# Performance work log

Hardware: AMD Instinct MI355X
Metric: run time of the kernel (lower is better)

The kernel has to match this reference:

```python
import jax, jax.numpy as jnp
import numpy as np

B, Wd, C, H, F = 48, 88, 256, 32, 1024
NH_SELF, NH_CROSS = 8, 8


def _ln(x, g, b, eps=1e-5):
    mu = x.mean(-1, keepdims=True)
    var = ((x - mu) ** 2).mean(-1, keepdims=True)
    return (x - mu) / jnp.sqrt(var + eps) * g + b


def setup_inputs() -> dict:
    key = jax.random.key(0)
    ks = jax.random.split(key, 16)
    s = 0.02  # weight init scale
    d = {
        'pooled_features': jax.random.normal(ks[0], (B, Wd, C), jnp.float32),
        'features': jax.random.normal(ks[1], (B, C, H, Wd), jnp.float32),
        'self_pe': jax.random.normal(ks[2], (Wd, C), jnp.float32),
        'cross_pe': jax.random.normal(ks[3], (H, C), jnp.float32),
    }
    # LayerNorm params
    for n in ['ln_qs', 'ln_vs', 'ln_qc', 'ln_kv', 'ln_vc', 'ln_ffn']:
        d[n + '_g'] = jnp.ones((C,), jnp.float32)
        d[n + '_b'] = jnp.zeros((C,), jnp.float32)
    # attention projections (stored [in,out]; y = x @ W + b)
    names = ['Wq_s', 'Wk_s', 'Wv_s', 'Wp_s', 'Wq_c', 'Wk_c', 'Wv_c', 'Wp_c']
    for i, n in enumerate(names):
        d[n] = jax.random.normal(ks[4 + i], (C, C), jnp.float32) * s
    for n in ['bq_s', 'bv_s', 'bp_s', 'bq_c', 'bv_c', 'bp_c']:
        d[n] = jnp.zeros((C,), jnp.float32)
    # FFN
    d['W1'] = jax.random.normal(ks[12], (C, F), jnp.float32) * s
    d['b1'] = jnp.zeros((F,), jnp.float32)
    d['W2'] = jax.random.normal(ks[13], (F, C), jnp.float32) * s
    d['b2'] = jnp.zeros((C,), jnp.float32)
    return d


def reference(pooled_features, features, self_pe, cross_pe,
              ln_qs_g, ln_qs_b, ln_vs_g, ln_vs_b,
              ln_qc_g, ln_qc_b, ln_kv_g, ln_kv_b, ln_vc_g, ln_vc_b,
              ln_ffn_g, ln_ffn_b,
              Wq_s, bq_s, Wk_s, Wv_s, bv_s, Wp_s, bp_s,
              Wq_c, bq_c, Wk_c, Wv_c, bv_c, Wp_c, bp_c,
              W1, b1, W2, b2):
    b, w, c = pooled_features.shape
    h = features.shape[2]
    ds = c // NH_SELF
    dc = c // NH_CROSS

    # ---- cross attention first (op_order='cross_first', with_pe=True) ----
    xq = pooled_features                                  # [B,W,C]
    qn = _ln(xq, ln_qc_g, ln_qc_b)
    kv = jnp.transpose(features, (0, 3, 2, 1))            # [B,W,H,C]
    kn = _ln(kv + cross_pe[None, None], ln_kv_g, ln_kv_b)
    vn = _ln(kv, ln_vc_g, ln_vc_b)
    q = (qn @ Wq_c + bq_c).reshape(b, w, NH_CROSS, dc)    # query len 1 per column
    k = (kn @ Wk_c).reshape(b, w, h, NH_CROSS, dc)
    v = (vn @ Wv_c + bv_c).reshape(b, w, h, NH_CROSS, dc)
    attn = jnp.einsum('bwhd,bwkhd->bwhk', q, k) * (dc ** -0.5)
    attn = jax.nn.softmax(attn, axis=-1)
    out = jnp.einsum('bwhk,bwkhd->bwhd', attn, v).reshape(b, w, c)
    x = out @ Wp_c + bp_c + xq

    # ---- self attention over width tokens ----
    qn = _ln(x + self_pe[None], ln_qs_g, ln_qs_b)
    vn = _ln(x, ln_vs_g, ln_vs_b)
    q = (qn @ Wq_s + bq_s).reshape(b, w, NH_SELF, ds)
    k = (qn @ Wk_s).reshape(b, w, NH_SELF, ds)
    v = (vn @ Wv_s + bv_s).reshape(b, w, NH_SELF, ds)
    attn = jnp.einsum('bnhd,bmhd->bhnm', q, k) * (ds ** -0.5)
    attn = jax.nn.softmax(attn, axis=-1)
    out = jnp.einsum('bhnm,bmhd->bnhd', attn, v).reshape(b, w, c)
    x = out @ Wp_s + bp_s + x

    # ---- FFN (mmcv FFN, num_fcs=2, GELU, identity residual) ----
    hdn = _ln(x, ln_ffn_g, ln_ffn_b)
    hdn = jax.nn.gelu(hdn @ W1 + b1, approximate=False) @ W2 + b2
    return x + hdn
```

## Files before the change

kernel.cpp:

```cpp
#include <hip/hip_runtime.h>
#include <math.h>

#define B_   48
#define W_   88
#define C_   256
#define H_   32
#define F_   1024
#define BW_  (B_ * W_)
#define BWH_ (B_ * W_ * H_)
#define HW_  (H_ * W_)

typedef float  f32x4  __attribute__((ext_vector_type(4)));
typedef __bf16 bf16x8 __attribute__((ext_vector_type(8)));

__device__ __forceinline__ unsigned short f2bf(float f) {
  union { float f; unsigned int u; } v; v.f = f;
  unsigned int r = v.u + 0x7FFFu + ((v.u >> 16) & 1u);
  return (unsigned short)(r >> 16);
}
__device__ __forceinline__ float bf2f(unsigned short h) {
  union { unsigned int u; float f; } v; v.u = ((unsigned int)h) << 16;
  return v.f;
}
__device__ __forceinline__ unsigned int pack2(float a, float b) {
  return (unsigned int)f2bf(a) | ((unsigned int)f2bf(b) << 16);
}

__global__ __launch_bounds__(256) void prep_all(
    const float* __restrict__ Wq_s, const float* __restrict__ Wk_s,
    const float* __restrict__ Wv_s, const float* __restrict__ Wp_s,
    const float* __restrict__ W1, const float* __restrict__ W2,
    const float* __restrict__ Wq_c, const float* __restrict__ Wk_c,
    const float* __restrict__ Wv_c, const float* __restrict__ Wp_c,
    const float* __restrict__ bq_s, const float* __restrict__ bv_s,
    const float* __restrict__ bq_c, const float* __restrict__ bv_c,
    const float* __restrict__ bp_c,
    const float* __restrict__ pooled, const float* __restrict__ cross_pe,
    const float* __restrict__ ln_qc_g, const float* __restrict__ ln_qc_b,
    unsigned short* __restrict__ wqkvs, unsigned short* __restrict__ wps,
    unsigned short* __restrict__ w1t, unsigned short* __restrict__ w2t,
    unsigned short* __restrict__ mqk, unsigned short* __restrict__ mvp,
    float* __restrict__ bqk, float* __restrict__ bvp,
    float* __restrict__ bqkvs, float* __restrict__ spe,
    unsigned short* __restrict__ qn_c) {
  __shared__ float smem[256 * 33 + 4 * 33];
  int blk = blockIdx.x, t = threadIdx.x;

  if (blk < 768) {
    const float* src; unsigned short* dst; int Cc, R, tile;
    if (blk < 64)       { src = Wq_s; dst = wqkvs;          Cc = 256;  R = 256;  tile = blk; }
    else if (blk < 128) { src = Wk_s; dst = wqkvs + 65536;  Cc = 256;  R = 256;  tile = blk - 64; }
    else if (blk < 192) { src = Wv_s; dst = wqkvs + 131072; Cc = 256;  R = 256;  tile = blk - 128; }
    else if (blk < 256) { src = Wp_s; dst = wps;            Cc = 256;  R = 256;  tile = blk - 192; }
    else if (blk < 512) { src = W1;   dst = w1t;            Cc = 1024; R = 256;  tile = blk - 256; }
    else                { src = W2;   dst = w2t;            Cc = 256;  R = 1024; tile = blk - 512; }
    int tcn = Cc >> 5;
    int tr = tile / tcn, tc = tile % tcn;
    float (*lds)[33] = (float(*)[33])smem;
    int r = t >> 3, c4 = (t & 7) * 4;
    float4 v = *(const float4*)(src + (size_t)(tr * 32 + r) * Cc + tc * 32 + c4);
    lds[r][c4 + 0] = v.x; lds[r][c4 + 1] = v.y; lds[r][c4 + 2] = v.z; lds[r][c4 + 3] = v.w;
    __syncthreads();
    int rd = t >> 3, cd4 = (t & 7) * 4;
    uint2 u;
    u.x = pack2(lds[cd4 + 0][rd], lds[cd4 + 1][rd]);
    u.y = pack2(lds[cd4 + 2][rd], lds[cd4 + 3][rd]);
    *(uint2*)(dst + (size_t)(tc * 32 + rd) * R + tr * 32 + cd4) = u;
  } else if (blk < 1280) {
    int lb = blk - 768;
    int h = lb >> 6, cb = lb & 63;
    float (*wq)[33] = (float(*)[33])smem;
    float (*wk)[33] = (float(*)[33])(smem + 256 * 33);
#pragma unroll
    for (int p = 0; p < 8; p++) {
      int dp = (t >> 3) + 32 * p, d4 = (t & 7) * 4;
      float4 v = *(const float4*)(Wq_c + (size_t)dp * 256 + 32 * h + d4);
      wq[dp][d4 + 0] = v.x; wq[dp][d4 + 1] = v.y; wq[dp][d4 + 2] = v.z; wq[dp][d4 + 3] = v.w;
    }
    if (t < 128) {
      int c_l = t >> 5, dd = t & 31;
      wk[c_l][dd] = Wk_c[(size_t)(cb * 4 + c_l) * 256 + 32 * h + dd];
    }
    __syncthreads();
    const float scale = 0.17677669529663689f;
    int c_l = t >> 6, ln = t & 63;
    int n = 256 * h + cb * 4 + c_l;
#pragma unroll
    for (int j = 0; j < 4; j++) {
      int dp = ln + 64 * j;
      float acc = 0.f;
#pragma unroll
      for (int dd = 0; dd < 32; dd++) acc += wq[dp][dd] * wk[c_l][dd];
      mqk[(size_t)n * 256 + dp] = f2bf(acc * scale);
    }
    if (ln == 0) {
      float bb = 0.f;
#pragma unroll
      for (int dd = 0; dd < 32; dd++) bb += bq_c[32 * h + dd] * wk[c_l][dd];
      bqk[n] = bb * scale;
    }
  } else if (blk < 1792) {
    int lb = blk - 1280;
    int h = lb >> 6, db = lb & 63;
    float (*wv)[33] = (float(*)[33])smem;
    float (*wp)[33] = (float(*)[33])(smem + 256 * 33);
#pragma unroll
    for (int p = 0; p < 8; p++) {
      int c = (t >> 3) + 32 * p, d4 = (t & 7) * 4;
      float4 v = *(const float4*)(Wv_c + (size_t)c * 256 + 32 * h + d4);
      wv[c][d4 + 0] = v.x; wv[c][d4 + 1] = v.y; wv[c][d4 + 2] = v.z; wv[c][d4 + 3] = v.w;
    }
    if (t < 128) {
      int d_l = t >> 5, dd = t & 31;
      wp[d_l][dd] = Wp_c[(size_t)(32 * h + dd) * 256 + db * 4 + d_l];
    }
    __syncthreads();
    int d_l = t >> 6, ln = t & 63;
    int d = db * 4 + d_l;
#pragma unroll
    for (int j = 0; j < 4; j++) {
      int c = ln + 64 * j;
      float acc = 0.f;
#pragma unroll
      for (int dd = 0; dd < 32; dd++) acc += wv[c][dd] * wp[d_l][dd];
      mvp[(size_t)d * 2048 + 256 * h + c] = f2bf(acc);
    }
  } else if (blk == 1792) {
    float acc = bp_c[t];
    for (int dp = 0; dp < 256; dp++) acc += bv_c[dp] * Wp_c[(size_t)dp * 256 + t];
    bvp[t] = acc;
    bqkvs[t] = bq_s[t]; bqkvs[256 + t] = 0.f; bqkvs[512 + t] = bv_s[t];
  } else if (blk == 1793) {
    int j = t >> 3, cp = t & 7;
    float sp = 0.f, sp2 = 0.f;
    for (int i = 0; i < 32; i++) {
      float v = cross_pe[j * 256 + cp * 32 + i];
      sp += v; sp2 += v * v;
    }
    smem[j * 8 + cp] = sp; smem[256 + j * 8 + cp] = sp2;
    __syncthreads();
    if (t < 32) {
      float a = 0.f, a2 = 0.f;
      for (int i = 0; i < 8; i++) { a += smem[t * 8 + i]; a2 += smem[256 + t * 8 + i]; }
      spe[t] = a; spe[32 + t] = a2;
    }
  } else {
    int row = blk - 1794, c = t;
    float v = pooled[(size_t)row * C_ + c];
    float s1 = v, s2 = v * v;
#pragma unroll
    for (int m = 32; m > 0; m >>= 1) {
      s1 += __shfl_xor(s1, m, 64); s2 += __shfl_xor(s2, m, 64);
    }
    float* red = smem;
    int wave = c >> 6;
    if ((c & 63) == 0) { red[wave] = s1; red[4 + wave] = s2; }
    __syncthreads();
    s1 = red[0] + red[1] + red[2] + red[3];
    s2 = red[4] + red[5] + red[6] + red[7];
    float mu = s1 * (1.f / C_);
    float rs = rsqrtf(s2 * (1.f / C_) - mu * mu + 1e-5f);
    qn_c[(size_t)row * C_ + c] = f2bf((v - mu) * rs * ln_qc_g[c] + ln_qc_b[c]);
  }
}

__global__ __launch_bounds__(704) void xattn_score(
    const float* __restrict__ features, const unsigned short* __restrict__ qt,
    const float* __restrict__ gk, const float* __restrict__ cross_pe,
    unsigned short* __restrict__ part1, float* __restrict__ pstat) {
  int b = blockIdx.x >> 4, ch = blockIdx.x & 15, c0 = ch * 16;
  __shared__ unsigned short kvl[2][16 * 8 * 88];
  __shared__ float pel[32][16];
  int t = threadIdx.x, w = t >> 3, head = t & 7;
  if (t < 512) {
    int j = t >> 4, c = t & 15;
    pel[j][c] = cross_pe[j * 256 + c0 + c];
  }
  float gq[16];
  {
    const unsigned short* qrow = qt + (size_t)(b * 88 + w) * 2048 + head * 256 + c0;
    bf16x8 q0 = *(const bf16x8*)qrow;
    bf16x8 q1 = *(const bf16x8*)(qrow + 8);
#pragma unroll
    for (int i = 0; i < 8; i++) {
      gq[i]     = gk[c0 + i]     * (float)q0[i];
      gq[8 + i] = gk[c0 + 8 + i] * (float)q1[i];
    }
  }
  const float* fbase = features + (size_t)(b * 256 + c0) * HW_;
  float4 rg[4];
  int iA[4];
  auto loadq = [&](int q) {
#pragma unroll
    for (int k = 0; k < 4; k++) {
      int p4 = t + k * 704;
      int c = p4 / 176, r = p4 - c * 176;
      int j8 = r / 22, w4 = (r - j8 * 22) * 4;
      iA[k] = c * 704 + j8 * 88 + w4;
      rg[k] = *(const float4*)(fbase + (size_t)c * HW_ + (q * 8 + j8) * 88 + w4);
    }
  };
  auto storeq = [&](int buf) {
#pragma unroll
    for (int k = 0; k < 4; k++) {
      uint2 u;
      u.x = pack2(rg[k].x, rg[k].y);
      u.y = pack2(rg[k].z, rg[k].w);
      *(uint2*)&kvl[buf][iA[k]] = u;
    }
  };
  unsigned short* dst = part1 + (size_t)((b * 16 + ch) * 88 + w) * 256;
  loadq(0); storeq(0);
  __syncthreads();
  for (int q = 0; q < 4; q++) {
    int cur = q & 1;
    if (q < 3) loadq(q + 1);
    const unsigned short* kb = kvl[cur];
    float a1q[8];
#pragma unroll
    for (int i = 0; i < 8; i++) a1q[i] = 0.f;
#pragma unroll
    for (int c = 0; c < 16; c++) {
      float g = gq[c];
      const unsigned short* row = kb + c * 704 + w;
#pragma unroll
      for (int j8 = 0; j8 < 8; j8++)
        a1q[j8] += g * (bf2f(row[j8 * 88]) + pel[q * 8 + j8][c]);
    }
    {
      float s1 = 0.f, s2 = 0.f, cr = 0.f;
#pragma unroll
      for (int c = 0; c < 16; c++) {
        float v = bf2f(kb[c * 704 + head * 88 + w]);
        s1 += v; s2 += v * v; cr += v * pel[q * 8 + head][c];
      }
      size_t sb = (size_t)(b * 16 + ch) * 3 * 2816 + (q * 8 + head) * 88 + w;
      pstat[sb] = s1; pstat[sb + 2816] = s2; pstat[sb + 5632] = cr;
    }
    {
      unsigned short pk[8];
#pragma unroll
      for (int i = 0; i < 8; i++) pk[i] = f2bf(a1q[i]);
      *(uint4*)(dst + q * 64 + head * 8) = *(uint4*)pk;
    }
    if (q < 3) storeq(cur ^ 1);
    __syncthreads();
  }
}

__global__ __launch_bounds__(256) void xattn_sm(
    const unsigned short* __restrict__ part1, const float* __restrict__ pstat,
    const unsigned short* __restrict__ qt, const float* __restrict__ spe,
    const float* __restrict__ gk, const float* __restrict__ bk,
    float* __restrict__ pr, float* __restrict__ s2a) {
  int bw = blockIdx.x, b = bw / 88, w = bw - b * 88;
  int t = threadIdx.x, head = t >> 5, j = t & 31;
  __shared__ float statl[3][32];
  int pidx = ((j >> 3) << 6) + head * 8 + (j & 7);
  float a1 = 0.f;
  for (int ch = 0; ch < 16; ch++)
    a1 += bf2f(part1[(size_t)((b * 16 + ch) * 88 + w) * 256 + pidx]);
  if (t < 96) {
    int s = t >> 5, jj = t & 31;
    float v = 0.f;
    for (int ch = 0; ch < 16; ch++)
      v += pstat[(size_t)(b * 16 + ch) * 3 * 2816 + s * 2816 + jj * 88 + w];
    statl[s][jj] = v;
  }
  __syncthreads();
  float s1 = statl[0][j], s2v = statl[1][j], cr = statl[2][j];
  float mu  = s1 * (1.f / 256.f);
  float rs  = rsqrtf(s2v * (1.f / 256.f) - mu * mu + 1e-5f);
  float muk = (s1 + spe[j]) * (1.f / 256.f);
  float rsk = rsqrtf((s2v + 2.f * cr + spe[32 + j]) * (1.f / 256.f) - muk * muk + 1e-5f);
  float a3 = 0.f, a4 = 0.f;
  {
    const unsigned short* qrow = qt + (size_t)bw * 2048 + head * 256 + j * 8;
#pragma unroll
    for (int i = 0; i < 8; i++) {
      int c = j * 8 + i;
      float qv = bf2f(qrow[i]);
      a3 += bk[c] * qv; a4 += gk[c] * qv;
    }
  }
#pragma unroll
  for (int m = 16; m > 0; m >>= 1) { a3 += __shfl_xor(a3, m, 32); a4 += __shfl_xor(a4, m, 32); }
  float s = rsk * a1 + a3 - muk * rsk * a4;
  float mx = s;
#pragma unroll
  for (int m = 16; m > 0; m >>= 1) mx = fmaxf(mx, __shfl_xor(mx, m, 32));
  float e = __expf(s - mx);
  float sum = e;
#pragma unroll
  for (int m = 16; m > 0; m >>= 1) sum += __shfl_xor(sum, m, 32);
  float p = e / sum;
  pr[((size_t)bw * 8 + head) * 32 + j] = p * rs;
  float sp = p * rs * mu;
#pragma unroll
  for (int m = 16; m > 0; m >>= 1) sp += __shfl_xor(sp, m, 32);
  if (j == 0) s2a[(size_t)bw * 8 + head] = sp;
}

__global__ __launch_bounds__(704) void xattn_ctx(
    const float* __restrict__ features, const float* __restrict__ pr,
    const float* __restrict__ s2a, const float* __restrict__ gv,
    const float* __restrict__ bvv, unsigned short* __restrict__ ctx) {
  int b = blockIdx.x >> 4, ch = blockIdx.x & 15, c0 = ch * 16;
  __shared__ unsigned short kvl[2][16 * 8 * 88];
  int t = threadIdx.x, w = t >> 3, head = t & 7;
  float S2 = s2a[(size_t)(b * 88 + w) * 8 + head];
  float U[16];
#pragma unroll
  for (int i = 0; i < 16; i++) U[i] = 0.f;

  const float* fbase = features + (size_t)(b * 256 + c0) * HW_;
  const float* prbase = pr + ((size_t)(b * 88 + w) * 8 + head) * 32;
  float4 rg[4];
  int iA[4];
  auto loadq = [&](int q) {
#pragma unroll
    for (int k = 0; k < 4; k++) {
      int p4 = t + k * 704;
      int c = p4 / 176, r = p4 - c * 176;
      int j8 = r / 22, w4 = (r - j8 * 22) * 4;
      iA[k] = c * 704 + j8 * 88 + w4;
      rg[k] = *(const float4*)(fbase + (size_t)c * HW_ + (q * 8 + j8) * 88 + w4);
    }
  };
  auto storeq = [&](int buf) {
#pragma unroll
    for (int k = 0; k < 4; k++) {
      uint2 u;
      u.x = pack2(rg[k].x, rg[k].y);
      u.y = pack2(rg[k].z, rg[k].w);
      *(uint2*)&kvl[buf][iA[k]] = u;
    }
  };
  loadq(0); storeq(0);
  __syncthreads();
  for (int q = 0; q < 4; q++) {
    int cur = q & 1;
    if (q < 3) loadq(q + 1);
    const unsigned short* kb = kvl[cur];
    float4 p0 = *(const float4*)(prbase + q * 8);
    float4 p1 = *(const float4*)(prbase + q * 8 + 4);
    float prr8[8] = {p0.x, p0.y, p0.z, p0.w, p1.x, p1.y, p1.z, p1.w};
#pragma unroll
    for (int c = 0; c < 16; c++) {
      const unsigned short* row = kb + c * 704 + w;
      float acc = U[c];
#pragma unroll
      for (int j8 = 0; j8 < 8; j8++)
        acc += prr8[j8] * bf2f(row[j8 * 88]);
      U[c] = acc;
    }
    if (q < 3) storeq(cur ^ 1);
    __syncthreads();
  }
  unsigned short* orow = ctx + (size_t)(b * 88 + w) * 2048 + head * 256 + c0;
  unsigned short pk[16];
#pragma unroll
  for (int i = 0; i < 16; i++)
    pk[i] = f2bf(gv[c0 + i] * (U[i] - S2) + bvv[c0 + i]);
  *(uint4*)(orow) = *(uint4*)pk;
  *(uint4*)(orow + 8) = *(uint4*)(pk + 8);
}

__global__ __launch_bounds__(256) void ln_rows(
    const float* __restrict__ x,
    const float* __restrict__ g, const float* __restrict__ bta,
    unsigned short* __restrict__ out) {
  int row = blockIdx.x, c = threadIdx.x;
  float v = x[(size_t)row * C_ + c];
  float s1 = v, s2 = v * v;
#pragma unroll
  for (int m = 32; m > 0; m >>= 1) {
    s1 += __shfl_xor(s1, m, 64);
    s2 += __shfl_xor(s2, m, 64);
  }
  __shared__ float red[8];
  int wave = c >> 6;
  if ((c & 63) == 0) { red[wave] = s1; red[4 + wave] = s2; }
  __syncthreads();
  s1 = red[0] + red[1] + red[2] + red[3];
  s2 = red[4] + red[5] + red[6] + red[7];
  float mu = s1 * (1.f / C_);
  float rs = rsqrtf(s2 * (1.f / C_) - mu * mu + 1e-5f);
  out[(size_t)row * C_ + c] = f2bf((v - mu) * rs * g[c] + bta[c]);
}

__global__ __launch_bounds__(256) void ln_dual(
    const float* __restrict__ x, const float* __restrict__ pe,
    const float* __restrict__ g1, const float* __restrict__ b1a,
    const float* __restrict__ g2, const float* __restrict__ b2a,
    unsigned short* __restrict__ out1, unsigned short* __restrict__ out2) {
  int row = blockIdx.x, c = threadIdx.x;
  float v = x[(size_t)row * C_ + c];
  float vp = v + pe[(size_t)(row % 88) * C_ + c];
  float s1 = v, s2 = v * v, t1 = vp, t2 = vp * vp;
#pragma unroll
  for (int m = 32; m > 0; m >>= 1) {
    s1 += __shfl_xor(s1, m, 64); s2 += __shfl_xor(s2, m, 64);
    t1 += __shfl_xor(t1, m, 64); t2 += __shfl_xor(t2, m, 64);
  }
  __shared__ float red[16];
  int wave = c >> 6;
  if ((c & 63) == 0) {
    red[wave] = s1; red[4 + wave] = s2; red[8 + wave] = t1; red[12 + wave] = t2;
  }
  __syncthreads();
  s1 = red[0] + red[1] + red[2] + red[3];
  s2 = red[4] + red[5] + red[6] + red[7];
  t1 = red[8] + red[9] + red[10] + red[11];
  t2 = red[12] + red[13] + red[14] + red[15];
  float mu = s1 * (1.f / C_), rs = rsqrtf(s2 * (1.f / C_) - mu * mu + 1e-5f);
  float mup = t1 * (1.f / C_), rsp = rsqrtf(t2 * (1.f / C_) - mup * mup + 1e-5f);
  out1[(size_t)row * C_ + c] = f2bf((vp - mup) * rsp * g1[c] + b1a[c]);
  out2[(size_t)row * C_ + c] = f2bf((v - mu) * rs * g2[c] + b2a[c]);
}

__global__ __launch_bounds__(256) void gemm_bt(
    const unsigned short* __restrict__ A, const unsigned short* __restrict__ Bt,
    int M, int N, int K,
    const float* __restrict__ bias, const float* __restrict__ resid,
    float* __restrict__ outF, unsigned short* __restrict__ outB, int act_gelu) {
  __shared__ __attribute__((aligned(16))) unsigned short As[64][32];
  __shared__ __attribute__((aligned(16))) unsigned short Bs[64][32];
  const int tiles_n = N >> 6;
  const int bm = blockIdx.x / tiles_n;
  const int bn = blockIdx.x % tiles_n;
  const int tid = threadIdx.x;
  const int wave = tid >> 6, lane = tid & 63;
  const int quad = lane >> 4, lr = lane & 15;
  const int wm = (wave >> 1) << 5, wn = (wave & 1) << 5;
  const int lrow = tid >> 2;
  const int lcol = (tid & 3) << 3;
  const size_t a_base = (size_t)(bm * 64 + lrow) * K + lcol;
  const size_t b_base = (size_t)(bn * 64 + lrow) * K + lcol;
  f32x4 acc[2][2] = {};
  uint4 areg = *(const uint4*)(A + a_base);
  uint4 breg = *(const uint4*)(Bt + b_base);
  for (int k0 = 0; k0 < K; k0 += 32) {
    *(uint4*)&As[lrow][lcol] = areg;
    *(uint4*)&Bs[lrow][lcol] = breg;
    __syncthreads();
    if (k0 + 32 < K) {
      areg = *(const uint4*)(A + a_base + k0 + 32);
      breg = *(const uint4*)(Bt + b_base + k0 + 32);
    }
    bf16x8 af0 = *(const bf16x8*)&As[wm + lr][quad << 3];
    bf16x8 af1 = *(const bf16x8*)&As[wm + 16 + lr][quad << 3];
    bf16x8 bf0 = *(const bf16x8*)&Bs[wn + lr][quad << 3];
    bf16x8 bf1 = *(const bf16x8*)&Bs[wn + 16 + lr][quad << 3];
    acc[0][0] = __builtin_amdgcn_mfma_f32_16x16x32_bf16(af0, bf0, acc[0][0], 0, 0, 0);
    acc[0][1] = __builtin_amdgcn_mfma_f32_16x16x32_bf16(af0, bf1, acc[0][1], 0, 0, 0);
    acc[1][0] = __builtin_amdgcn_mfma_f32_16x16x32_bf16(af1, bf0, acc[1][0], 0, 0, 0);
    acc[1][1] = __builtin_amdgcn_mfma_f32_16x16x32_bf16(af1, bf1, acc[1][1], 0, 0, 0);
    __syncthreads();
  }
#pragma unroll
  for (int i = 0; i < 2; i++)
#pragma unroll
    for (int j = 0; j < 2; j++)
#pragma unroll
      for (int rr = 0; rr < 4; rr++) {
        int row = bm * 64 + wm + i * 16 + quad * 4 + rr;
        int col = bn * 64 + wn + j * 16 + lr;
        float val = acc[i][j][rr];
        if (bias) val += bias[col];
        if (act_gelu) val = 0.5f * val * (1.f + erff(val * 0.70710678118654752f));
        if (resid) val += resid[(size_t)row * N + col];
        if (outF) outF[(size_t)row * N + col] = val;
        else outB[(size_t)row * N + col] = f2bf(val);
      }
}

__global__ __launch_bounds__(256) void gemm_bt_st(
    const unsigned short* __restrict__ A, const unsigned short* __restrict__ Bt,
    int M, int N, int K, int ldc,
    const float* __restrict__ bias, float* __restrict__ outF) {
  __shared__ __attribute__((aligned(16))) unsigned short As[64][32];
  __shared__ __attribute__((aligned(16))) unsigned short Bs[64][32];
  const int tiles_n = N >> 6;
  const int bm = blockIdx.x / tiles_n;
  const int bn = blockIdx.x % tiles_n;
  const int tid = threadIdx.x;
  const int wave = tid >> 6, lane = tid & 63;
  const int quad = lane >> 4, lr = lane & 15;
  const int wm = (wave >> 1) << 5, wn = (wave & 1) << 5;
  const int lrow = tid >> 2;
  const int lcol = (tid & 3) << 3;
  const size_t a_base = (size_t)(bm * 64 + lrow) * K + lcol;
  const size_t b_base = (size_t)(bn * 64 + lrow) * K + lcol;
  f32x4 acc[2][2] = {};
  uint4 areg = *(const uint4*)(A + a_base);
  uint4 breg = *(const uint4*)(Bt + b_base);
  for (int k0 = 0; k0 < K; k0 += 32) {
    *(uint4*)&As[lrow][lcol] = areg;
    *(uint4*)&Bs[lrow][lcol] = breg;
    __syncthreads();
    if (k0 + 32 < K) {
      areg = *(const uint4*)(A + a_base + k0 + 32);
      breg = *(const uint4*)(Bt + b_base + k0 + 32);
    }
    bf16x8 af0 = *(const bf16x8*)&As[wm + lr][quad << 3];
    bf16x8 af1 = *(const bf16x8*)&As[wm + 16 + lr][quad << 3];
    bf16x8 bf0 = *(const bf16x8*)&Bs[wn + lr][quad << 3];
    bf16x8 bf1 = *(const bf16x8*)&Bs[wn + 16 + lr][quad << 3];
    acc[0][0] = __builtin_amdgcn_mfma_f32_16x16x32_bf16(af0, bf0, acc[0][0], 0, 0, 0);
    acc[0][1] = __builtin_amdgcn_mfma_f32_16x16x32_bf16(af0, bf1, acc[0][1], 0, 0, 0);
    acc[1][0] = __builtin_amdgcn_mfma_f32_16x16x32_bf16(af1, bf0, acc[1][0], 0, 0, 0);
    acc[1][1] = __builtin_amdgcn_mfma_f32_16x16x32_bf16(af1, bf1, acc[1][1], 0, 0, 0);
    __syncthreads();
  }
#pragma unroll
  for (int i = 0; i < 2; i++)
#pragma unroll
    for (int j = 0; j < 2; j++)
#pragma unroll
      for (int rr = 0; rr < 4; rr++) {
        int row = bm * 64 + wm + i * 16 + quad * 4 + rr;
        int col = bn * 64 + wn + j * 16 + lr;
        outF[(size_t)row * ldc + col] = acc[i][j][rr] + bias[col];
      }
}

__global__ __launch_bounds__(192) void self_attn3(
    const float* __restrict__ qkv, unsigned short* __restrict__ out) {
  int b = blockIdx.x >> 3;
  int h = blockIdx.x & 7;
  int t = threadIdx.x;
  __shared__ float kl[88][33];
  __shared__ float vl[88][33];
  for (int i = t; i < 704; i += 192) {
    int m = i >> 3, d4 = (i & 7) << 2;
    float4 kv4 = *(const float4*)(qkv + (size_t)(b * 88 + m) * 768 + 256 + h * 32 + d4);
    float4 vv4 = *(const float4*)(qkv + (size_t)(b * 88 + m) * 768 + 512 + h * 32 + d4);
    kl[m][d4 + 0] = kv4.x; kl[m][d4 + 1] = kv4.y; kl[m][d4 + 2] = kv4.z; kl[m][d4 + 3] = kv4.w;
    vl[m][d4 + 0] = vv4.x; vl[m][d4 + 1] = vv4.y; vl[m][d4 + 2] = vv4.z; vl[m][d4 + 3] = vv4.w;
  }
  __syncthreads();
  int r = t >> 1, dh = t & 1;
  if (r < 88) {
    const float* qrow = qkv + (size_t)(b * 88 + r) * 768 + h * 32;
    float qr[32];
#pragma unroll
    for (int g = 0; g < 8; g++) {
      float4 q4 = *(const float4*)(qrow + g * 4);
      qr[g * 4 + 0] = q4.x; qr[g * 4 + 1] = q4.y; qr[g * 4 + 2] = q4.z; qr[g * 4 + 3] = q4.w;
    }
    float sreg[44];
    float mx = -1e30f;
    int m0 = dh * 44;
    for (int mi = 0; mi < 44; mi++) {
      const float* krow = kl[m0 + mi];
      float s = 0.f;
#pragma unroll
      for (int d = 0; d < 32; d++) s += qr[d] * krow[d];
      s *= 0.17677669529663689f;
      sreg[mi] = s;
      mx = fmaxf(mx, s);
    }
    mx = fmaxf(mx, __shfl_xor(mx, 1, 64));
    float sum = 0.f;
    for (int mi = 0; mi < 44; mi++) { float e = __expf(sreg[mi] - mx); sreg[mi] = e; sum += e; }
    sum += __shfl_xor(sum, 1, 64);
    float inv = 1.f / sum;
    float o[32];
#pragma unroll
    for (int d = 0; d < 32; d++) o[d] = 0.f;
    for (int mi = 0; mi < 44; mi++) {
      float p = sreg[mi] * inv;
      const float* vrow = vl[m0 + mi];
#pragma unroll
      for (int d = 0; d < 32; d++) o[d] += p * vrow[d];
    }
#pragma unroll
    for (int d = 0; d < 32; d++) o[d] += __shfl_xor(o[d], 1, 64);
    unsigned short* orow = out + (size_t)(b * 88 + r) * 256 + h * 32 + dh * 16;
    uint4 u0, u1;
    int d0 = dh * 16;
    u0.x = pack2(o[d0 + 0], o[d0 + 1]);  u0.y = pack2(o[d0 + 2], o[d0 + 3]);
    u0.z = pack2(o[d0 + 4], o[d0 + 5]);  u0.w = pack2(o[d0 + 6], o[d0 + 7]);
    u1.x = pack2(o[d0 + 8], o[d0 + 9]);  u1.y = pack2(o[d0 + 10], o[d0 + 11]);
    u1.z = pack2(o[d0 + 12], o[d0 + 13]); u1.w = pack2(o[d0 + 14], o[d0 + 15]);
    *(uint4*)(orow) = u0;
    *(uint4*)(orow + 8) = u1;
  }
}

extern "C" void kernel_launch(void* const* d_in, const int* in_sizes, int n_in,
                              void* d_out, int out_size, void* d_ws, size_t ws_size,
                              hipStream_t stream) {
  (void)in_sizes; (void)n_in; (void)out_size; (void)ws_size;
  const float* pooled   = (const float*)d_in[0];
  const float* features = (const float*)d_in[1];
  const float* self_pe  = (const float*)d_in[2];
  const float* cross_pe = (const float*)d_in[3];
  const float* ln_qs_g = (const float*)d_in[4],  *ln_qs_b = (const float*)d_in[5];
  const float* ln_vs_g = (const float*)d_in[6],  *ln_vs_b = (const float*)d_in[7];
  const float* ln_qc_g = (const float*)d_in[8],  *ln_qc_b = (const float*)d_in[9];
  const float* ln_kv_g = (const float*)d_in[10], *ln_kv_b = (const float*)d_in[11];
  const float* ln_vc_g = (const float*)d_in[12], *ln_vc_b = (const float*)d_in[13];
  const float* ln_ffn_g = (const float*)d_in[14], *ln_ffn_b = (const float*)d_in[15];
  const float* Wq_s = (const float*)d_in[16], *Wk_s = (const float*)d_in[17];
  const float* Wv_s = (const float*)d_in[18], *Wp_s = (const float*)d_in[19];
  const float* Wq_c = (const float*)d_in[20], *Wk_c = (const float*)d_in[21];
  const float* Wv_c = (const float*)d_in[22], *Wp_c = (const float*)d_in[23];
  const float* bq_s = (const float*)d_in[24], *bv_s = (const float*)d_in[25];
  const float* bp_s = (const float*)d_in[26], *bq_c = (const float*)d_in[27];
  const float* bv_c = (const float*)d_in[28], *bp_c = (const float*)d_in[29];
  const float* W1 = (const float*)d_in[30], *b1 = (const float*)d_in[31];
  const float* W2 = (const float*)d_in[32], *b2 = (const float*)d_in[33];
  float* outp = (float*)d_out;
  char* ws = (char*)d_ws;

  size_t off = 0;
  auto alloc = [&](size_t bytes) { size_t o = off; off = (off + bytes + 255) & ~(size_t)255; return o; };
  size_t QT   = alloc((size_t)BW_ * 2048 * 2);
  size_t CTX  = alloc((size_t)BW_ * 2048 * 2);
  size_t MQK  = alloc((size_t)2048 * 256 * 2);
  size_t MVP  = alloc((size_t)256 * 2048 * 2);
  size_t BQK  = alloc(2048 * 4);
  size_t BVP  = alloc(256 * 4);
  size_t WQKVS = alloc((size_t)768 * 256 * 2);
  size_t BQKVS = alloc(768 * 4);
  size_t WPS = alloc(65536 * 2);
  size_t W1T = alloc(262144 * 2), W2T = alloc(262144 * 2);
  size_t QN_C = alloc((size_t)BW_ * C_ * 2);
  size_t SPE  = alloc(64 * 4);
  size_t PART1 = alloc((size_t)48 * 16 * 88 * 256 * 2);
  size_t PSTAT = alloc((size_t)48 * 16 * 3 * 2816 * 4);
  size_t PRB   = alloc((size_t)BW_ * 256 * 4);
  size_t S2A   = alloc((size_t)BW_ * 8 * 4);
  size_t offp = PART1;
  auto allocP = [&](size_t bytes) { size_t o = offp; offp = (offp + bytes + 255) & ~(size_t)255; return o; };
  size_t X1    = allocP((size_t)BW_ * C_ * 4);
  size_t QN_S  = allocP((size_t)BW_ * C_ * 2);
  size_t VN_S  = allocP((size_t)BW_ * C_ * 2);
  size_t QKV_S = allocP((size_t)BW_ * 768 * 4);
  size_t S_O   = allocP((size_t)BW_ * C_ * 2);
  size_t X2    = allocP((size_t)BW_ * C_ * 4);
  size_t FFN   = allocP((size_t)BW_ * C_ * 2);
  size_t H1    = allocP((size_t)BW_ * F_ * 2);

  unsigned short* qtp  = (unsigned short*)(ws + QT);
  unsigned short* ctx  = (unsigned short*)(ws + CTX);
  unsigned short* mqk  = (unsigned short*)(ws + MQK);
  unsigned short* mvp  = (unsigned short*)(ws + MVP);
  float* bqk = (float*)(ws + BQK);
  float* bvp = (float*)(ws + BVP);
  unsigned short* wqkvs = (unsigned short*)(ws + WQKVS);
  float* bqkvs = (float*)(ws + BQKVS);
  unsigned short* wps = (unsigned short*)(ws + WPS);
  unsigned short* w1t = (unsigned short*)(ws + W1T), *w2t = (unsigned short*)(ws + W2T);
  unsigned short* qn_c = (unsigned short*)(ws + QN_C);
  float* spe   = (float*)(ws + SPE);
  unsigned short* part1 = (unsigned short*)(ws + PART1);
  float* pstat = (float*)(ws + PSTAT);
  float* prb   = (float*)(ws + PRB);
  float* s2a   = (float*)(ws + S2A);
  float*          x1   = (float*)(ws + X1);
  unsigned short* qn_s = (unsigned short*)(ws + QN_S);
  unsigned short* vn_s = (unsigned short*)(ws + VN_S);
  float* qkv_s = (float*)(ws + QKV_S);
  unsigned short* s_o  = (unsigned short*)(ws + S_O);
  float*          x2   = (float*)(ws + X2);
  unsigned short* ffn_n = (unsigned short*)(ws + FFN);
  unsigned short* h1    = (unsigned short*)(ws + H1);

  prep_all<<<6018, 256, 0, stream>>>(
      Wq_s, Wk_s, Wv_s, Wp_s, W1, W2, Wq_c, Wk_c, Wv_c, Wp_c,
      bq_s, bv_s, bq_c, bv_c, bp_c, pooled, cross_pe, ln_qc_g, ln_qc_b,
      wqkvs, wps, w1t, w2t, mqk, mvp, bqk, bvp, bqkvs, spe, qn_c);

  gemm_bt<<<(BW_ / 64) * (2048 / 64), 256, 0, stream>>>(qn_c, mqk, BW_, 2048, 256,
      bqk, nullptr, nullptr, qtp, 0);

  xattn_score<<<768, 704, 0, stream>>>(features, qtp, ln_kv_g, cross_pe, part1, pstat);
  xattn_sm<<<BW_, 256, 0, stream>>>(part1, pstat, qtp, spe, ln_kv_g, ln_kv_b, prb, s2a);
  xattn_ctx<<<768, 704, 0, stream>>>(features, prb, s2a, ln_vc_g, ln_vc_b, ctx);

  gemm_bt<<<(BW_ / 64) * (C_ / 64), 256, 0, stream>>>(ctx, mvp, BW_, C_, 2048,
      bvp, pooled, x1, nullptr, 0);

  ln_dual<<<BW_, 256, 0, stream>>>(x1, self_pe, ln_qs_g, ln_qs_b,
                                   ln_vs_g, ln_vs_b, qn_s, vn_s);

  gemm_bt_st<<<(BW_ / 64) * (512 / 64), 256, 0, stream>>>(qn_s, wqkvs, BW_, 512, 256,
      768, bqkvs, qkv_s);
  gemm_bt_st<<<(BW_ / 64) * (256 / 64), 256, 0, stream>>>(vn_s, wqkvs + 131072, BW_, 256, 256,
      768, bqkvs + 512, qkv_s + 512);

  self_attn3<<<B_ * 8, 192, 0, stream>>>(qkv_s, s_o);

  gemm_bt<<<(BW_ / 64) * (C_ / 64), 256, 0, stream>>>(s_o, wps, BW_, C_, C_,
      bp_s, x1, x2, nullptr, 0);

  ln_rows<<<BW_, 256, 0, stream>>>(x2, ln_ffn_g, ln_ffn_b, ffn_n);
  gemm_bt<<<(BW_ / 64) * (F_ / 64), 256, 0, stream>>>(ffn_n, w1t, BW_, F_, C_,
      b1, nullptr, nullptr, h1, 1);
  gemm_bt<<<(BW_ / 64) * (C_ / 64), 256, 0, stream>>>(h1, w2t, BW_, C_, F_,
      b2, x2, outp, nullptr, 0);
}
```

Measured before the change: 581.1 us.

## Fuse cross-attention score, softmax and context kernels into one width-tiled kernel

Replaces the three cross-attention kernels (channel-chunked score partials, softmax reduction, context accumulation) with a single kernel in which each block owns one batch and eight width columns and loops over all channels itself. This removes the partial-score and statistics buffers in global memory, their reduction kernel and two launches. In exchange, features are read twice per block with no double buffering, only 528 blocks of 256 threads run, and each block is serialized over channels.

New measurement: 557.0 us. 1.04x faster.

```diff
diff --git a/kernel.cpp b/kernel.cpp
--- a/kernel.cpp
+++ b/kernel.cpp
@@ -164,206 +164,159 @@
   }
 }
 
-__global__ __launch_bounds__(704) void xattn_score(
+#define CSTR 258
+__global__ __launch_bounds__(256) void xfuse(
     const float* __restrict__ features, const unsigned short* __restrict__ qt,
-    const float* __restrict__ gk, const float* __restrict__ cross_pe,
-    unsigned short* __restrict__ part1, float* __restrict__ pstat) {
-  int b = blockIdx.x >> 4, ch = blockIdx.x & 15, c0 = ch * 16;
-  __shared__ unsigned short kvl[2][16 * 8 * 88];
-  __shared__ float pel[32][16];
-  int t = threadIdx.x, w = t >> 3, head = t & 7;
-  if (t < 512) {
-    int j = t >> 4, c = t & 15;
-    pel[j][c] = cross_pe[j * 256 + c0 + c];
-  }
-  float gq[16];
+    const float* __restrict__ gk, const float* __restrict__ bk,
+    const float* __restrict__ cross_pe, const float* __restrict__ spe,
+    const float* __restrict__ gv, const float* __restrict__ bvv,
+    unsigned short* __restrict__ ctx) {
+  int b = blockIdx.x / 11, wo = blockIdx.x % 11;
+  int t = threadIdx.x;
+  int w = t >> 5, h = (t >> 2) & 7, jo = t & 3;
+  int ws = t >> 5, js = t & 31;
+  int gw = wo * 8 + w;
+
+  __shared__ __attribute__((aligned(16))) unsigned short kvl[32 * CSTR];
+  __shared__ float pel[32 * 32];
+  __shared__ float qgl[8 * 264];
+  __shared__ float psl[8 * 264];
+  __shared__ float mukl[8][32], rskl[8][32], mul[8][32], rsl[8][32];
+  __shared__ float s2hl[8][8];
+
+  float a1q[8] = {0.f, 0.f, 0.f, 0.f, 0.f, 0.f, 0.f, 0.f};
+  float st1 = 0.f, st2 = 0.f, scr = 0.f;
+  float a3p = 0.f, a4p = 0.f;
+
+  for (int ch = 0; ch < 8; ch++) {
+#pragma unroll
+    for (int k = 0; k < 4; k++) {
+      int s = t + k * 256;
+      int c = s >> 5, j = s & 31;
+      const float* src = features + ((size_t)(b * 256 + ch * 32 + c)) * HW_ + j * 88 + wo * 8;
+      float4 v0 = *(const float4*)(src);
+      float4 v1 = *(const float4*)(src + 4);
+      unsigned short* dst = &kvl[c * CSTR + j];
+      dst[0]   = f2bf(v0.x); dst[32]  = f2bf(v0.y); dst[64]  = f2bf(v0.z); dst[96]  = f2bf(v0.w);
+      dst[128] = f2bf(v1.x); dst[160] = f2bf(v1.y); dst[192] = f2bf(v1.z); dst[224] = f2bf(v1.w);
+    }
+#pragma unroll
+    for (int k = 0; k < 4; k++) {
+      int s = t + k * 256;
+      int c = s >> 5, j = s & 31;
+      pel[c * 32 + j] = cross_pe[j * 256 + ch * 32 + c];
+    }
+    {
+      int c0 = ch * 32 + jo * 8;
+      bf16x8 qv = *(const bf16x8*)(qt + (size_t)(b * 88 + gw) * 2048 + h * 256 + c0);
+      float4 g0 = *(const float4*)(gk + c0), g1 = *(const float4*)(gk + c0 + 4);
+      float4 b0 = *(const float4*)(bk + c0), b1 = *(const float4*)(bk + c0 + 4);
+      float ga[8] = {g0.x, g0.y, g0.z, g0.w, g1.x, g1.y, g1.z, g1.w};
+      float ba[8] = {b0.x, b0.y, b0.z, b0.w, b1.x, b1.y, b1.z, b1.w};
+#pragma unroll
+      for (int i = 0; i < 8; i++) {
+        float qf = (float)qv[i];
+        qgl[w * 264 + h * 33 + jo * 8 + i] = ga[i] * qf;
+        a3p += ba[i] * qf;
+        a4p += ga[i] * qf;
+      }
+    }
+    __syncthreads();
+#pragma unroll 4
+    for (int c = 0; c < 32; c++) {
+      float gq = qgl[w * 264 + h * 33 + c];
+      const unsigned short* kr = &kvl[c * CSTR + w * 32 + jo * 8];
+      const float* pr_ = &pel[c * 32 + jo * 8];
+#pragma unroll
+      for (int i = 0; i < 8; i++)
+        a1q[i] += gq * (bf2f(kr[i]) + pr_[i]);
+    }
+#pragma unroll 4
+    for (int c = 0; c < 32; c++) {
+      float v = bf2f(kvl[c * CSTR + ws * 32 + js]);
+      float p = pel[c * 32 + js];
+      st1 += v; st2 += v * v; scr += v * p;
+    }
+    __syncthreads();
+  }
+
   {
-    const unsigned short* qrow = qt + (size_t)(b * 88 + w) * 2048 + head * 256 + c0;
-    bf16x8 q0 = *(const bf16x8*)qrow;
-    bf16x8 q1 = *(const bf16x8*)(qrow + 8);
+    float mu  = st1 * (1.f / 256.f);
+    float rs  = rsqrtf(st2 * (1.f / 256.f) - mu * mu + 1e-5f);
+    float muk = (st1 + spe[js]) * (1.f / 256.f);
+    float rsk = rsqrtf((st2 + 2.f * scr + spe[32 + js]) * (1.f / 256.f) - muk * muk + 1e-5f);
+    mukl[ws][js] = muk; rskl[ws][js] = rsk; mul[ws][js] = mu; rsl[ws][js] = rs;
+  }
+  a3p += __shfl_xor(a3p, 1, 64); a3p += __shfl_xor(a3p, 2, 64);
+  a4p += __shfl_xor(a4p, 1, 64); a4p += __shfl_xor(a4p, 2, 64);
+  __syncthreads();
+
+  {
+    float s8[8];
+    float mx = -1e30f;
 #pragma unroll
     for (int i = 0; i < 8; i++) {
-      gq[i]     = gk[c0 + i]     * (float)q0[i];
-      gq[8 + i] = gk[c0 + 8 + i] * (float)q1[i];
-    }
-  }
-  const float* fbase = features + (size_t)(b * 256 + c0) * HW_;
-  float4 rg[4];
-  int iA[4];
-  auto loadq = [&](int q) {
+      int j = jo * 8 + i;
+      float rsk = rskl[w][j];
+      float s = rsk * a1q[i] + a3p - mukl[w][j] * rsk * a4p;
+      s8[i] = s; mx = fmaxf(mx, s);
+    }
+    mx = fmaxf(mx, __shfl_xor(mx, 1, 64));
+    mx = fmaxf(mx, __shfl_xor(mx, 2, 64));
+    float sum = 0.f;
+#pragma unroll
+    for (int i = 0; i < 8; i++) { s8[i] = __expf(s8[i] - mx); sum += s8[i]; }
+    sum += __shfl_xor(sum, 1, 64); sum += __shfl_xor(sum, 2, 64);
+    float inv = 1.f / sum;
+    float sp = 0.f;
+#pragma unroll
+    for (int i = 0; i < 8; i++) {
+      int j = jo * 8 + i;
+      float prs = s8[i] * inv * rsl[w][j];
+      psl[w * 264 + h * 33 + j] = prs;
+      sp += prs * mul[w][j];
+    }
+    sp += __shfl_xor(sp, 1, 64); sp += __shfl_xor(sp, 2, 64);
+    if (jo == 0) s2hl[w][h] = sp;
+  }
+  __syncthreads();
+
+  float S2 = s2hl[w][h];
+  for (int ch = 0; ch < 8; ch++) {
 #pragma unroll
     for (int k = 0; k < 4; k++) {
-      int p4 = t + k * 704;
-      int c = p4 / 176, r = p4 - c * 176;
-      int j8 = r / 22, w4 = (r - j8 * 22) * 4;
-      iA[k] = c * 704 + j8 * 88 + w4;
-      rg[k] = *(const float4*)(fbase + (size_t)c * HW_ + (q * 8 + j8) * 88 + w4);
-    }
-  };
-  auto storeq = [&](int buf) {
-#pragma unroll
-    for (int k = 0; k < 4; k++) {
-      uint2 u;
-      u.x = pack2(rg[k].x, rg[k].y);
-      u.y = pack2(rg[k].z, rg[k].w);
-      *(uint2*)&kvl[buf][iA[k]] = u;
-    }
-  };
-  unsigned short* dst = part1 + (size_t)((b * 16 + ch) * 88 + w) * 256;
-  loadq(0); storeq(0);
-  __syncthreads();
-  for (int q = 0; q < 4; q++) {
-    int cur = q & 1;
-    if (q < 3) loadq(q + 1);
-    const unsigned short* kb = kvl[cur];
-    float a1q[8];
-#pragma unroll
-    for (int i = 0; i < 8; i++) a1q[i] = 0.f;
-#pragma unroll
-    for (int c = 0; c < 16; c++) {
-      float g = gq[c];
-      const unsigned short* row = kb + c * 704 + w;
-#pragma unroll
-      for (int j8 = 0; j8 < 8; j8++)
-        a1q[j8] += g * (bf2f(row[j8 * 88]) + pel[q * 8 + j8][c]);
-    }
-    {
-      float s1 = 0.f, s2 = 0.f, cr = 0.f;
-#pragma unroll
-      for (int c = 0; c < 16; c++) {
-        float v = bf2f(kb[c * 704 + head * 88 + w]);
-        s1 += v; s2 += v * v; cr += v * pel[q * 8 + head][c];
-      }
-      size_t sb = (size_t)(b * 16 + ch) * 3 * 2816 + (q * 8 + head) * 88 + w;
-      pstat[sb] = s1; pstat[sb + 2816] = s2; pstat[sb + 5632] = cr;
-    }
-    {
-      unsigned short pk[8];
-#pragma unroll
-      for (int i = 0; i < 8; i++) pk[i] = f2bf(a1q[i]);
-      *(uint4*)(dst + q * 64 + head * 8) = *(uint4*)pk;
-    }
-    if (q < 3) storeq(cur ^ 1);
-    __syncthreads();
-  }
-}
-
-__global__ __launch_bounds__(256) void xattn_sm(
-    const unsigned short* __restrict__ part1, const float* __restrict__ pstat,
-    const unsigned short* __restrict__ qt, const float* __restrict__ spe,
-    const float* __restrict__ gk, const float* __restrict__ bk,
-    float* __restrict__ pr, float* __restrict__ s2a) {
-  int bw = blockIdx.x, b = bw / 88, w = bw - b * 88;
-  int t = threadIdx.x, head = t >> 5, j = t & 31;
-  __shared__ float statl[3][32];
-  int pidx = ((j >> 3) << 6) + head * 8 + (j & 7);
-  float a1 = 0.f;
-  for (int ch = 0; ch < 16; ch++)
-    a1 += bf2f(part1[(size_t)((b * 16 + ch) * 88 + w) * 256 + pidx]);
-  if (t < 96) {
-    int s = t >> 5, jj = t & 31;
-    float v = 0.f;
-    for (int ch = 0; ch < 16; ch++)
-      v += pstat[(size_t)(b * 16 + ch) * 3 * 2816 + s * 2816 + jj * 88 + w];
-    statl[s][jj] = v;
-  }
-  __syncthreads();
-  float s1 = statl[0][j], s2v = statl[1][j], cr = statl[2][j];
-  float mu  = s1 * (1.f / 256.f);
-  float rs  = rsqrtf(s2v * (1.f / 256.f) - mu * mu + 1e-5f);
-  float muk = (s1 + spe[j]) * (1.f / 256.f);
-  float rsk = rsqrtf((s2v + 2.f * cr + spe[32 + j]) * (1.f / 256.f) - muk * muk + 1e-5f);
-  float a3 = 0.f, a4 = 0.f;
-  {
-    const unsigned short* qrow = qt + (size_t)bw * 2048 + head * 256 + j * 8;
-#pragma unroll
-    for (int i = 0; i < 8; i++) {
-      int c = j * 8 + i;
-      float qv = bf2f(qrow[i]);
-      a3 += bk[c] * qv; a4 += gk[c] * qv;
-    }
-  }
-#pragma unroll
-  for (int m = 16; m > 0; m >>= 1) { a3 += __shfl_xor(a3, m, 32); a4 += __shfl_xor(a4, m, 32); }
-  float s = rsk * a1 + a3 - muk * rsk * a4;
-  float mx = s;
-#pragma unroll
-  for (int m = 16; m > 0; m >>= 1) mx = fmaxf(mx, __shfl_xor(mx, m, 32));
-  float e = __expf(s - mx);
-  float sum = e;
-#pragma unroll
-  for (int m = 16; m > 0; m >>= 1) sum += __shfl_xor(sum, m, 32);
-  float p = e / sum;
-  pr[((size_t)bw * 8 + head) * 32 + j] = p * rs;
-  float sp = p * rs * mu;
-#pragma unroll
-  for (int m = 16; m > 0; m >>= 1) sp += __shfl_xor(sp, m, 32);
-  if (j == 0) s2a[(size_t)bw * 8 + head] = sp;
-}
-
-__global__ __launch_bounds__(704) void xattn_ctx(
-    const float* __restrict__ features, const float* __restrict__ pr,
-    const float* __restrict__ s2a, const float* __restrict__ gv,
-    const float* __restrict__ bvv, unsigned short* __restrict__ ctx) {
-  int b = blockIdx.x >> 4, ch = blockIdx.x & 15, c0 = ch * 16;
-  __shared__ unsigned short kvl[2][16 * 8 * 88];
-  int t = threadIdx.x, w = t >> 3, head = t & 7;
-  float S2 = s2a[(size_t)(b * 88 + w) * 8 + head];
-  float U[16];
-#pragma unroll
-  for (int i = 0; i < 16; i++) U[i] = 0.f;
-
-  const float* fbase = features + (size_t)(b * 256 + c0) * HW_;
-  const float* prbase = pr + ((size_t)(b * 88 + w) * 8 + head) * 32;
-  float4 rg[4];
-  int iA[4];
-  auto loadq = [&](int q) {
-#pragma unroll
-    for (int k = 0; k < 4; k++) {
-      int p4 = t + k * 704;
-      int c = p4 / 176, r = p4 - c * 176;
-      int j8 = r / 22, w4 = (r - j8 * 22) * 4;
-      iA[k] = c * 704 + j8 * 88 + w4;
-      rg[k] = *(const float4*)(fbase + (size_t)c * HW_ + (q * 8 + j8) * 88 + w4);
-    }
-  };
-  auto storeq = [&](int buf) {
-#pragma unroll
-    for (int k = 0; k < 4; k++) {
-      uint2 u;
-      u.x = pack2(rg[k].x, rg[k].y);
-      u.y = pack2(rg[k].z, rg[k].w);
-      *(uint2*)&kvl[buf][iA[k]] = u;
-    }
-  };
-  loadq(0); storeq(0);
-  __syncthreads();
-  for (int q = 0; q < 4; q++) {
-    int cur = q & 1;
-    if (q < 3) loadq(q + 1);
-    const unsigned short* kb = kvl[cur];
-    float4 p0 = *(const float4*)(prbase + q * 8);
-    float4 p1 = *(const float4*)(prbase + q * 8 + 4);
-    float prr8[8] = {p0.x, p0.y, p0.z, p0.w, p1.x, p1.y, p1.z, p1.w};
-#pragma unroll
-    for (int c = 0; c < 16; c++) {
-      const unsigned short* row = kb + c * 704 + w;
-      float acc = U[c];
-#pragma unroll
-      for (int j8 = 0; j8 < 8; j8++)
-        acc += prr8[j8] * bf2f(row[j8 * 88]);
-      U[c] = acc;
-    }
-    if (q < 3) storeq(cur ^ 1);
-    __syncthreads();
-  }
-  unsigned short* orow = ctx + (size_t)(b * 88 + w) * 2048 + head * 256 + c0;
-  unsigned short pk[16];
-#pragma unroll
-  for (int i = 0; i < 16; i++)
-    pk[i] = f2bf(gv[c0 + i] * (U[i] - S2) + bvv[c0 + i]);
-  *(uint4*)(orow) = *(uint4*)pk;
-  *(uint4*)(orow + 8) = *(uint4*)(pk + 8);
+      int s = t + k * 256;
+      int c = s >> 5, j = s & 31;
+      const float* src = features + ((size_t)(b * 256 + ch * 32 + c)) * HW_ + j * 88 + wo * 8;
+      float4 v0 = *(const float4*)(src);
+      float4 v1 = *(const float4*)(src + 4);
+      unsigned short* dst = &kvl[c * CSTR + j];
+      dst[0]   = f2bf(v0.x); dst[32]  = f2bf(v0.y); dst[64]  = f2bf(v0.z); dst[96]  = f2bf(v0.w);
+      dst[128] = f2bf(v1.x); dst[160] = f2bf(v1.y); dst[192] = f2bf(v1.z); dst[224] = f2bf(v1.w);
+    }
+    __syncthreads();
+    float U[8] = {0.f, 0.f, 0.f, 0.f, 0.f, 0.f, 0.f, 0.f};
+    const float* pp = &psl[w * 264 + h * 33];
+#pragma unroll 4
+    for (int j = 0; j < 32; j++) {
+      float p = pp[j];
+      const unsigned short* kr = &kvl[jo * 8 * CSTR + w * 32 + j];
+#pragma unroll
+      for (int i = 0; i < 8; i++)
+        U[i] += p * bf2f(kr[i * CSTR]);
+    }
+    int c0 = ch * 32 + jo * 8;
+    float4 gv0 = *(const float4*)(gv + c0), gv1 = *(const float4*)(gv + c0 + 4);
+    float4 bv0 = *(const float4*)(bvv + c0), bv1 = *(const float4*)(bvv + c0 + 4);
+    float gva[8] = {gv0.x, gv0.y, gv0.z, gv0.w, gv1.x, gv1.y, gv1.z, gv1.w};
+    float bva[8] = {bv0.x, bv0.y, bv0.z, bv0.w, bv1.x, bv1.y, bv1.z, bv1.w};
+    unsigned short pk[8];
+#pragma unroll
+    for (int i = 0; i < 8; i++)
+      pk[i] = f2bf(gva[i] * (U[i] - S2) + bva[i]);
+    *(uint4*)(ctx + (size_t)(b * 88 + gw) * 2048 + h * 256 + c0) = *(uint4*)pk;
+    if (ch < 7) __syncthreads();
+  }
 }
 
 __global__ __launch_bounds__(256) void ln_rows(
@@ -629,20 +582,14 @@
   size_t W1T = alloc(262144 * 2), W2T = alloc(262144 * 2);
   size_t QN_C = alloc((size_t)BW_ * C_ * 2);
   size_t SPE  = alloc(64 * 4);
-  size_t PART1 = alloc((size_t)48 * 16 * 88 * 256 * 2);
-  size_t PSTAT = alloc((size_t)48 * 16 * 3 * 2816 * 4);
-  size_t PRB   = alloc((size_t)BW_ * 256 * 4);
-  size_t S2A   = alloc((size_t)BW_ * 8 * 4);
-  size_t offp = PART1;
-  auto allocP = [&](size_t bytes) { size_t o = offp; offp = (offp + bytes + 255) & ~(size_t)255; return o; };
-  size_t X1    = allocP((size_t)BW_ * C_ * 4);
-  size_t QN_S  = allocP((size_t)BW_ * C_ * 2);
-  size_t VN_S  = allocP((size_t)BW_ * C_ * 2);
-  size_t QKV_S = allocP((size_t)BW_ * 768 * 4);
-  size_t S_O   = allocP((size_t)BW_ * C_ * 2);
-  size_t X2    = allocP((size_t)BW_ * C_ * 4);
-  size_t FFN   = allocP((size_t)BW_ * C_ * 2);
-  size_t H1    = allocP((size_t)BW_ * F_ * 2);
+  size_t X1    = alloc((size_t)BW_ * C_ * 4);
+  size_t QN_S  = alloc((size_t)BW_ * C_ * 2);
+  size_t VN_S  = alloc((size_t)BW_ * C_ * 2);
+  size_t QKV_S = alloc((size_t)BW_ * 768 * 4);
+  size_t S_O   = alloc((size_t)BW_ * C_ * 2);
+  size_t X2    = alloc((size_t)BW_ * C_ * 4);
+  size_t FFN   = alloc((size_t)BW_ * C_ * 2);
+  size_t H1    = alloc((size_t)BW_ * F_ * 2);
 
   unsigned short* qtp  = (unsigned short*)(ws + QT);
   unsigned short* ctx  = (unsigned short*)(ws + CTX);
@@ -656,10 +603,6 @@
   unsigned short* w1t = (unsigned short*)(ws + W1T), *w2t = (unsigned short*)(ws + W2T);
   unsigned short* qn_c = (unsigned short*)(ws + QN_C);
   float* spe   = (float*)(ws + SPE);
-  unsigned short* part1 = (unsigned short*)(ws + PART1);
-  float* pstat = (float*)(ws + PSTAT);
-  float* prb   = (float*)(ws + PRB);
-  float* s2a   = (float*)(ws + S2A);
   float*          x1   = (float*)(ws + X1);
   unsigned short* qn_s = (unsigned short*)(ws + QN_S);
   unsigned short* vn_s = (unsigned short*)(ws + VN_S);
@@ -677,9 +620,8 @@
   gemm_bt<<<(BW_ / 64) * (2048 / 64), 256, 0, stream>>>(qn_c, mqk, BW_, 2048, 256,
       bqk, nullptr, nullptr, qtp, 0);
 
-  xattn_score<<<768, 704, 0, stream>>>(features, qtp, ln_kv_g, cross_pe, part1, pstat);
-  xattn_sm<<<BW_, 256, 0, stream>>>(part1, pstat, qtp, spe, ln_kv_g, ln_kv_b, prb, s2a);
-  xattn_ctx<<<768, 704, 0, stream>>>(features, prb, s2a, ln_vc_g, ln_vc_b, ctx);
+  xfuse<<<B_ * 11, 256, 0, stream>>>(features, qtp, ln_kv_g, ln_kv_b,
+      cross_pe, spe, ln_vc_g, ln_vc_b, ctx);
 
   gemm_bt<<<(BW_ / 64) * (C_ / 64), 256, 0, stream>>>(ctx, mvp, BW_, C_, 2048,
       bvp, pooled, x1, nullptr, 0);
```
